# Optimization experiments

Hardware: AMD Instinct MI355X
Metric: run time of the kernel (lower is better)

The kernel has to match this reference:

```python
import jax, jax.numpy as jnp
import numpy as np

Lc, Lq = 20, 50
CTX, CTXM = 2048, 512
NEG = -1e30


def setup_inputs() -> dict:
    key = jax.random.key(0)
    ks = jax.random.split(key, 8)
    B = 2048
    Vid_enc = jax.random.normal(ks[0], (B, Lc, CTX), dtype=jnp.float32)
    Ques_enc = jax.random.normal(ks[1], (B, CTXM, Lq), dtype=jnp.float32)
    V_mask = jnp.ones((B, Lc), dtype=jnp.float32)
    Q_mask = jnp.ones((B, Lq), dtype=jnp.float32)
    # weight-normed Linear(2048 -> 512): v [out,in], g [out], b [out]
    trans_v = jax.random.normal(ks[2], (CTXM, CTX), dtype=jnp.float32) * 0.02
    trans_g = jnp.linalg.norm(trans_v, axis=1)  # matches torch weight_norm init
    trans_b = jnp.zeros((CTXM,), dtype=jnp.float32)
    w4V = jax.random.normal(ks[3], (CTXM, 1), dtype=jnp.float32) * 0.05
    w4Q = jax.random.normal(ks[4], (CTXM, 1), dtype=jnp.float32) * 0.05
    w4mlu = jax.random.normal(ks[5], (1, 1, CTXM), dtype=jnp.float32) * 0.05
    bias = jnp.zeros((1,), dtype=jnp.float32)
    return {
        "Vid_enc": Vid_enc, "Ques_enc": Ques_enc,
        "V_mask": V_mask, "Q_mask": Q_mask,
        "trans_v": trans_v, "trans_g": trans_g, "trans_b": trans_b,
        "w4V": w4V, "w4Q": w4Q, "w4mlu": w4mlu, "bias": bias,
    }


def reference(Vid_enc, Ques_enc, V_mask, Q_mask,
              trans_v, trans_g, trans_b, w4V, w4Q, w4mlu, bias):
    # weight-normed linear projection: W = g * v / ||v||_row
    W = trans_g[:, None] * trans_v / jnp.linalg.norm(trans_v, axis=1, keepdims=True)
    V = jnp.einsum('blc,mc->blm', Vid_enc, W) + trans_b          # [B,Lc,512]
    Q = jnp.swapaxes(Ques_enc, 1, 2)                             # [B,Lq,512]
    # trilinear similarity (dropout p inactive at inference)
    s0 = V @ w4V                                                 # [B,Lc,1]
    s1 = jnp.swapaxes(Q @ w4Q, 1, 2)                             # [B,1,Lq]
    s2 = jnp.einsum('bld,bqd->blq', V * w4mlu, Q)                # [B,Lc,Lq]
    S = s0 + s1 + s2 + bias                                      # [B,Lc,Lq]
    Vm = V_mask[:, :, None]                                      # [B,Lc,1]
    Qm = Q_mask[:, None, :]                                      # [B,1,Lq]
    S1 = jax.nn.softmax(S * Qm + (1.0 - Qm) * NEG, axis=2)
    S2 = jax.nn.softmax(S * Vm + (1.0 - Vm) * NEG, axis=1)
    A = jnp.einsum('blq,bqd->bld', S1, Q)                        # [B,Lc,512]
    Bt = jnp.einsum('blq,bmq->blm', S1, S2)                      # [B,Lc,Lc]
    Bv = jnp.einsum('blm,bmd->bld', Bt, V)                       # [B,Lc,512]
    out = jnp.concatenate([V, A, V * A, V * Bv], axis=2)         # [B,Lc,2048]
    return jnp.swapaxes(out, 1, 2)                               # [B,2048,Lc]
```

## Files before the change

### kernel.cpp

```cpp
#include <hip/hip_runtime.h>
#include <math.h>

#define B_    2048
#define LC    20
#define LQ    50
#define CTX   2048
#define CTXM  512
#define NEGV  -1e30f

typedef __fp16 half8 __attribute__((ext_vector_type(8)));
typedef __fp16 f16x2 __attribute__((ext_vector_type(2)));
typedef float f32x4  __attribute__((ext_vector_type(4)));
typedef unsigned int uint;

__device__ __forceinline__ half8 cvt8v(float4 a, float4 b) {
    union { f16x2 h[4]; half8 v; } r;
    r.h[0] = __builtin_amdgcn_cvt_pkrtz(a.x, a.y);
    r.h[1] = __builtin_amdgcn_cvt_pkrtz(a.z, a.w);
    r.h[2] = __builtin_amdgcn_cvt_pkrtz(b.x, b.y);
    r.h[3] = __builtin_amdgcn_cvt_pkrtz(b.z, b.w);
    return r.v;
}
__device__ __forceinline__ half8 cvt8(const float* x) {
    union { f16x2 h[4]; half8 v; } r;
    r.h[0] = __builtin_amdgcn_cvt_pkrtz(x[0], x[1]);
    r.h[1] = __builtin_amdgcn_cvt_pkrtz(x[2], x[3]);
    r.h[2] = __builtin_amdgcn_cvt_pkrtz(x[4], x[5]);
    r.h[3] = __builtin_amdgcn_cvt_pkrtz(x[6], x[7]);
    return r.v;
}

#define GLOAD_LDS16(g, l)                                                        \
    __builtin_amdgcn_global_load_lds(                                            \
        (const __attribute__((address_space(1))) unsigned int*)(g),              \
        (__attribute__((address_space(3))) unsigned int*)(l), 16, 0, 0)

__global__ __launch_bounds__(256)
void scale_kernel(const float* __restrict__ trans_v,
                  const float* __restrict__ trans_g,
                  float* __restrict__ scale) {
    int m = blockIdx.x;
    int t = threadIdx.x;
    const float* row = trans_v + (size_t)m * CTX;
    float ss = 0.f;
    for (int i = t; i < CTX; i += 256) { float v = row[i]; ss += v * v; }
    __shared__ float red[256];
    red[t] = ss;
    __syncthreads();
    for (int s = 128; s > 0; s >>= 1) {
        if (t < s) red[t] += red[t + s];
        __syncthreads();
    }
    if (t == 0) scale[m] = trans_g[m] / sqrtf(red[0]);
}

__global__ __launch_bounds__(256)
void bpack_kernel(const float* __restrict__ Wt,
                  const float* __restrict__ scale,
                  char* __restrict__ Bp) {
    int u = blockIdx.x * 256 + threadIdx.x;
    int o = u * 16;
    int nslab  = o >> 20;
    int rem    = o & 1048575;
    int kchunk = rem >> 14;
    int rem2   = rem & 16383;
    int rpair  = rem2 >> 7;
    int cphys  = rem2 & 127;
    int clog   = cphys ^ ((rpair & 7) << 4);
    int rsub   = clog >> 6;
    int k0     = kchunk * 32 + ((clog & 63) >> 1);
    int n      = nslab * 256 + rpair * 2 + rsub;
    float s = scale[n];
    const float* wr = Wt + (size_t)n * CTX + k0;
    union { __fp16 h[8]; uint4 u4; } out;
#pragma unroll
    for (int e = 0; e < 8; e++) out.h[e] = (__fp16)(wr[e] * s);
    *(uint4*)&Bp[o] = out.u4;
}

__global__ __launch_bounds__(512, 4)
void gemm_kernel(const float* __restrict__ A,
                 const char*  __restrict__ Bp,
                 const float* __restrict__ trans_b,
                 float* __restrict__ V)
{
    __shared__ char lds[49152] __attribute__((aligned(16)));

    int t = threadIdx.x;
    int orig = blockIdx.x;
    int wg = (orig & 7) * 80 + (orig >> 3);
    int nslab = wg & 1;
    int m0 = (wg >> 1) * 128;
    int n0 = nslab << 8;

    int wid = t >> 6, lane = t & 63;
    int l15 = lane & 15;
    int q16 = (lane >> 4) << 4;
    int ksl = lane >> 4;
    int rq  = (lane >> 4) << 2;
    int wm = (wid >> 2) << 6;
    int wn = (wid & 3) << 6;

    int r_a = t >> 2;
    int sl  = t & 3;
    int a_dst = 32768 + sl * 2048 + r_a * 16;
    const float* arow = A + (size_t)(m0 + r_a) * CTX + sl * 8;

    const char* bslab = Bp + (size_t)nslab * (64 * 16384);

    f32x4 acc[4][4];
#pragma unroll
    for (int i = 0; i < 4; i++)
#pragma unroll
        for (int j = 0; j < 4; j++) acc[i][j] = (f32x4){0.f, 0.f, 0.f, 0.f};

    {
        const char* src = bslab + t * 16;
#pragma unroll
        for (int i = 0; i < 2; i++)
            GLOAD_LDS16(src + i * 8192, lds + i * 8192 + t * 16);
    }
    float4 ra0 = *(const float4*)arow;
    float4 ra1 = *(const float4*)(arow + 4);

    int cur = 0;
    for (int it = 0; it < 64; ++it) {
        *(half8*)&lds[a_dst + cur * 8192] = cvt8v(ra0, ra1);
        __syncthreads();

        if (it + 1 < 64) {
            const char* src = bslab + (size_t)(it + 1) * 16384 + t * 16;
            char* dst = lds + (cur ^ 1) * 16384 + t * 16;
#pragma unroll
            for (int i = 0; i < 2; i++)
                GLOAD_LDS16(src + i * 8192, dst + i * 8192);
            ra0 = *(const float4*)(arow + (it + 1) * 32);
            ra1 = *(const float4*)(arow + (it + 1) * 32 + 4);
        }

        const char* Bb = lds + cur * 16384;
        const char* Ab = lds + 32768 + cur * 8192;
        half8 af[4];
#pragma unroll
        for (int mt = 0; mt < 4; mt++)
            af[mt] = *(const half8*)&Ab[ksl * 2048 + (wm + mt * 16 + l15) * 16];
#pragma unroll
        for (int nt = 0; nt < 4; nt++) {
            int r  = wn + nt * 16 + l15;
            int rp = r >> 1;
            int c  = (r & 1) * 64 + q16;
            half8 bh = *(const half8*)&Bb[rp * 128 + (c ^ ((rp & 7) << 4))];
#pragma unroll
            for (int mt = 0; mt < 4; mt++)
                acc[mt][nt] = __builtin_amdgcn_mfma_f32_16x16x32_f16(af[mt], bh, acc[mt][nt], 0, 0, 0);
        }
        cur ^= 1;
    }

#pragma unroll
    for (int nt = 0; nt < 4; nt++) {
        int col = n0 + wn + nt * 16 + l15;
        float tb = trans_b[col];
#pragma unroll
        for (int mt = 0; mt < 4; mt++) {
            int m = m0 + wm + mt * 16 + rq;
#pragma unroll
            for (int rg = 0; rg < 4; rg++)
                V[(size_t)(m + rg) * CTXM + col] = acc[mt][nt][rg] + tb;
        }
    }
}

__global__ __launch_bounds__(512, 2)
void attn_kernel(const float* __restrict__ Ques,
                 const float* __restrict__ V_mask,
                 const float* __restrict__ Q_mask,
                 const float* __restrict__ w4V,
                 const float* __restrict__ w4Q,
                 const float* __restrict__ w4mlu,
                 const float* __restrict__ bias,
                 const float* __restrict__ V,
                 float* __restrict__ out)
{
    __shared__ __fp16 Qs[512 * 56 + 8];
    __shared__ float Ssh[LC][LQ];
    __shared__ float S1f[LC][LQ];
    __shared__ float S2f[LC][LQ];
    __shared__ __fp16 S1h[LC][72];
    __shared__ __fp16 S1l[LC][72];
    __shared__ __fp16 Bth[LC][40];
    __shared__ __fp16 Btl[LC][40];
    __shared__ float s1p[8][LQ];
    __shared__ float s0sh[LC];
    __shared__ float s1qsh[LQ];
    __shared__ float qmsh[LQ];
    __shared__ float vmsh[LC];

    int b = blockIdx.x;
    int t = threadIdx.x;
    int wid = t >> 6, lane = t & 63;
    int l15 = lane & 15;
    int kq  = (lane >> 4) << 3;
    int rq  = (lane >> 4) << 2;
    const float* Qb = Ques + (size_t)b * (CTXM * LQ);
    const float* Vb = V + (size_t)b * (LC * CTXM);

    if (t < LQ) qmsh[t] = Q_mask[(size_t)b * LQ + t];
    else if (t >= 64 && t < 64 + LC) vmsh[t - 64] = V_mask[(size_t)b * LC + (t - 64)];
    if (t < 8) Qs[512 * 56 + t] = (__fp16)0;

#pragma unroll
    for (int i = 0; i < 7; i++) {
        int task = t + 512 * i;
        int d  = task / 7;
        int sc = task - d * 7;
        const float* qr = Qb + (size_t)d * LQ + sc * 8;
        float xs[8];
        if (sc < 6) {
            float2 p0 = *(const float2*)&qr[0];
            float2 p1 = *(const float2*)&qr[2];
            float2 p2 = *(const float2*)&qr[4];
            float2 p3 = *(const float2*)&qr[6];
            xs[0] = p0.x; xs[1] = p0.y; xs[2] = p1.x; xs[3] = p1.y;
            xs[4] = p2.x; xs[5] = p2.y; xs[6] = p3.x; xs[7] = p3.y;
        } else {
            float2 p0 = *(const float2*)&qr[0];
            xs[0] = p0.x; xs[1] = p0.y;
            xs[2] = 0.f; xs[3] = 0.f; xs[4] = 0.f; xs[5] = 0.f;
            xs[6] = 0.f; xs[7] = 0.f;
        }
        *(half8*)&Qs[d * 56 + sc * 8] = cvt8(xs);
    }

    for (int l = wid; l < LC; l += 8) {
        float a = 0.f;
        const float* vr = Vb + (size_t)l * CTXM;
#pragma unroll
        for (int i = 0; i < CTXM / 64; i++)
            a = fmaf(vr[lane + 64 * i], w4V[lane + 64 * i], a);
#pragma unroll
        for (int o = 32; o > 0; o >>= 1) a += __shfl_xor(a, o);
        if (lane == 0) s0sh[l] = a;
    }
    __syncthreads();

    {
        int q = (lane < LQ) ? lane : (LQ - 1);
        float a = 0.f;
#pragma unroll
        for (int i = 0; i < 64; i++) {
            int d = (wid << 6) + i;
            a = fmaf((float)Qs[d * 56 + q], w4Q[d], a);
        }
        if (lane < LQ) s1p[wid][lane] = a;
    }

    int mt = wid >> 2, nt = wid & 3;
    f32x4 accS = {0.f, 0.f, 0.f, 0.f};
    {
        int lA = mt * 16 + l15; if (lA > LC - 1) lA = LC - 1;
        int qB = nt * 16 + l15; if (qB > LQ - 1) qB = LQ - 1;
        const float* vrow = Vb + (size_t)lA * CTXM;
        for (int kt = 0; kt < 16; kt++) {
            int d0 = kt * 32 + kq;
            float xa[8];
            float4 va = *(const float4*)&vrow[d0];
            float4 vc = *(const float4*)&vrow[d0 + 4];
            float4 wa = *(const float4*)&w4mlu[d0];
            float4 wc = *(const float4*)&w4mlu[d0 + 4];
            xa[0] = va.x * wa.x; xa[1] = va.y * wa.y; xa[2] = va.z * wa.z; xa[3] = va.w * wa.w;
            xa[4] = vc.x * wc.x; xa[5] = vc.y * wc.y; xa[6] = vc.z * wc.z; xa[7] = vc.w * wc.w;
            half8 vf = cvt8(xa);
            union { __fp16 h[8]; half8 v; } qq;
#pragma unroll
            for (int e = 0; e < 8; e++) qq.h[e] = Qs[(d0 + e) * 56 + qB];
            accS = __builtin_amdgcn_mfma_f32_16x16x32_f16(vf, qq.v, accS, 0, 0, 0);
        }
    }
    __syncthreads();

    if (t < LQ) {
        float s = 0.f;
#pragma unroll
        for (int w = 0; w < 8; w++) s += s1p[w][t];
        s1qsh[t] = s;
    }
    __syncthreads();

    {
        float bb = bias[0];
        int q = nt * 16 + l15;
#pragma unroll
        for (int r = 0; r < 4; r++) {
            int l = mt * 16 + rq + r;
            if (l < LC && q < LQ)
                Ssh[l][q] = accS[r] + s0sh[l] + s1qsh[q] + bb;
        }
    }
    __syncthreads();

    for (int l = wid; l < LC; l += 8) {
        float x;
        if (lane < LQ) {
            float qm = qmsh[lane];
            x = Ssh[l][lane] * qm + (1.f - qm) * NEGV;
        } else x = -INFINITY;
        float mx = x;
#pragma unroll
        for (int o = 32; o > 0; o >>= 1) mx = fmaxf(mx, __shfl_xor(mx, o));
        float e = (lane < LQ) ? expf(x - mx) : 0.f;
        float sum = e;
#pragma unroll
        for (int o = 32; o > 0; o >>= 1) sum += __shfl_xor(sum, o);
        float p = e / sum;
        if (lane < LQ) S1f[l][lane] = p;
        __fp16 hs = (__fp16)p;
        __fp16 ls = (__fp16)(p - (float)hs);
        S1h[l][lane] = (lane < LQ) ? hs : (__fp16)0;
        S1l[l][lane] = (lane < LQ) ? ls : (__fp16)0;
    }

    for (int ci = 0; ci < 7; ci++) {
        int c = wid * 7 + ci;
        if (c < LQ) {
            float x;
            if (lane < LC) {
                float vm = vmsh[lane];
                x = Ssh[lane][c] * vm + (1.f - vm) * NEGV;
            } else x = -INFINITY;
            float mx = x;
#pragma unroll
            for (int o = 32; o > 0; o >>= 1) mx = fmaxf(mx, __shfl_xor(mx, o));
            float e = (lane < LC) ? expf(x - mx) : 0.f;
            float sum = e;
#pragma unroll
            for (int o = 32; o > 0; o >>= 1) sum += __shfl_xor(sum, o);
            if (lane < LC) S2f[lane][c] = e / sum;
        }
    }
    __syncthreads();

    if (t < LC * LC) {
        int l = t % LC, m = t / LC;
        float s = 0.f;
#pragma unroll
        for (int j = 0; j < LQ; j++) s = fmaf(S1f[l][j], S2f[m][j], s);
        __fp16 hs = (__fp16)s;
        Bth[l][m] = hs;
        Btl[l][m] = (__fp16)(s - (float)hs);
    }
    if (t < 240) {
        int l = t % LC, m = LC + t / LC;
        Bth[l][m] = (__fp16)0; Btl[l][m] = (__fp16)0;
    }
    __syncthreads();

    float* outb = out + (size_t)b * (4 * CTXM * LC);
#pragma unroll 1
    for (int i = 0; i < 4; i++) {
        int dt = wid + 8 * i;
        int d0 = dt * 16;
        int dq = d0 + l15;
        half8 qf0 = *(const half8*)&Qs[dq * 56 + kq];
        half8 qf1 = *(const half8*)&Qs[dq * 56 + 32 + kq];
        float xv[8];
#pragma unroll
        for (int e = 0; e < 8; e++) {
            int m = kq + e;
            int mc = (m < LC) ? m : 0;
            float vv = Vb[(size_t)mc * CTXM + d0 + l15];
            xv[e] = (m < LC) ? vv : 0.f;
        }
        half8 vt = cvt8(xv);

        f32x4 accA[2] = {{0.f,0.f,0.f,0.f},{0.f,0.f,0.f,0.f}};
        f32x4 accB[2] = {{0.f,0.f,0.f,0.f},{0.f,0.f,0.f,0.f}};
#pragma unroll
        for (int n2 = 0; n2 < 2; n2++) {
            int lS = n2 * 16 + l15; if (lS > LC - 1) lS = LC - 1;
            half8 s1h0 = *(const half8*)&S1h[lS][kq];
            half8 s1l0 = *(const half8*)&S1l[lS][kq];
            half8 s1h1 = *(const half8*)&S1h[lS][32 + kq];
            half8 s1l1 = *(const half8*)&S1l[lS][32 + kq];
            accA[n2] = __builtin_amdgcn_mfma_f32_16x16x32_f16(qf0, s1h0, accA[n2], 0, 0, 0);
            accA[n2] = __builtin_amdgcn_mfma_f32_16x16x32_f16(qf0, s1l0, accA[n2], 0, 0, 0);
            accA[n2] = __builtin_amdgcn_mfma_f32_16x16x32_f16(qf1, s1h1, accA[n2], 0, 0, 0);
            accA[n2] = __builtin_amdgcn_mfma_f32_16x16x32_f16(qf1, s1l1, accA[n2], 0, 0, 0);
            half8 bh = *(const half8*)&Bth[lS][kq];
            half8 bl = *(const half8*)&Btl[lS][kq];
            accB[n2] = __builtin_amdgcn_mfma_f32_16x16x32_f16(vt, bh, accB[n2], 0, 0, 0);
            accB[n2] = __builtin_amdgcn_mfma_f32_16x16x32_f16(vt, bl, accB[n2], 0, 0, 0);
        }

#pragma unroll
        for (int n2 = 0; n2 < 2; n2++) {
            int l = n2 * 16 + l15;
            if (l < LC) {
#pragma unroll
                for (int r = 0; r < 4; r++) {
                    int d = d0 + rq + r;
                    float vv = Vb[(size_t)l * CTXM + d];
                    float a  = accA[n2][r];
                    float bv = accB[n2][r];
                    size_t base = (size_t)d * LC + l;
                    outb[base]                 = vv;
                    outb[base + CTXM * LC]     = a;
                    outb[base + 2 * CTXM * LC] = vv * a;
                    outb[base + 3 * CTXM * LC] = vv * bv;
                }
            }
        }
    }
}

extern "C" void kernel_launch(void* const* d_in, const int* in_sizes, int n_in,
                              void* d_out, int out_size, void* d_ws, size_t ws_size,
                              hipStream_t stream) {
    const float* Vid   = (const float*)d_in[0];
    const float* Ques  = (const float*)d_in[1];
    const float* Vmask = (const float*)d_in[2];
    const float* Qmask = (const float*)d_in[3];
    const float* tv    = (const float*)d_in[4];
    const float* tg    = (const float*)d_in[5];
    const float* tb    = (const float*)d_in[6];
    const float* w4V   = (const float*)d_in[7];
    const float* w4Q   = (const float*)d_in[8];
    const float* w4mlu = (const float*)d_in[9];
    const float* bias  = (const float*)d_in[10];
    float* out = (float*)d_out;

    float* scale = (float*)d_ws;
    float* V     = scale + 512;
    char*  Bp    = (char*)(V + (size_t)40960 * 512);

    scale_kernel<<<512, 256, 0, stream>>>(tv, tg, scale);
    bpack_kernel<<<512, 256, 0, stream>>>(tv, scale, Bp);
    gemm_kernel<<<640, 512, 0, stream>>>(Vid, Bp, tb, V);
    attn_kernel<<<B_, 512, 0, stream>>>(Ques, Vmask, Qmask, w4V, w4Q, w4mlu, bias, V, out);
}
```

Before: 401.0 us.

## Unroll GEMM k-loop by two with explicit vmcnt waits and raw barriers

Rewrites the projection GEMM main loop to process two k-steps per iteration with fixed LDS buffer offsets. It replaces __syncthreads with s_barrier plus explicit s_waitcnt vmcnt(2), so async global-to-LDS loads for the next stage stay in flight across the barrier instead of being fully drained. The A-tile register prefetch now reaches one stage further ahead. The hand-counted waits depend on the exact order of memory ops, which makes the code fragile if the compiler reorders loads.

```diff
diff --git a/kernel.cpp b/kernel.cpp
--- a/kernel.cpp
+++ b/kernel.cpp
@@ -116,45 +116,83 @@
 
     {
         const char* src = bslab + t * 16;
-#pragma unroll
-        for (int i = 0; i < 2; i++)
-            GLOAD_LDS16(src + i * 8192, lds + i * 8192 + t * 16);
-    }
-    float4 ra0 = *(const float4*)arow;
-    float4 ra1 = *(const float4*)(arow + 4);
-
-    int cur = 0;
-    for (int it = 0; it < 64; ++it) {
-        *(half8*)&lds[a_dst + cur * 8192] = cvt8v(ra0, ra1);
-        __syncthreads();
-
-        if (it + 1 < 64) {
-            const char* src = bslab + (size_t)(it + 1) * 16384 + t * 16;
-            char* dst = lds + (cur ^ 1) * 16384 + t * 16;
-#pragma unroll
-            for (int i = 0; i < 2; i++)
-                GLOAD_LDS16(src + i * 8192, dst + i * 8192);
-            ra0 = *(const float4*)(arow + (it + 1) * 32);
-            ra1 = *(const float4*)(arow + (it + 1) * 32 + 4);
-        }
-
-        const char* Bb = lds + cur * 16384;
-        const char* Ab = lds + 32768 + cur * 8192;
-        half8 af[4];
-#pragma unroll
-        for (int mt = 0; mt < 4; mt++)
-            af[mt] = *(const half8*)&Ab[ksl * 2048 + (wm + mt * 16 + l15) * 16];
-#pragma unroll
-        for (int nt = 0; nt < 4; nt++) {
-            int r  = wn + nt * 16 + l15;
-            int rp = r >> 1;
-            int c  = (r & 1) * 64 + q16;
-            half8 bh = *(const half8*)&Bb[rp * 128 + (c ^ ((rp & 7) << 4))];
+        GLOAD_LDS16(src, lds + t * 16);
+        GLOAD_LDS16(src + 8192, lds + 8192 + t * 16);
+    }
+    float4 rAe0 = *(const float4*)(arow);
+    float4 rAe1 = *(const float4*)(arow + 4);
+    float4 rAo0 = *(const float4*)(arow + 32);
+    float4 rAo1 = *(const float4*)(arow + 36);
+
+    for (int ii = 0; ii < 32; ++ii) {
+        int t0 = ii * 2;
+        *(half8*)&lds[a_dst] = cvt8v(rAe0, rAe1);
+        asm volatile("s_waitcnt vmcnt(2)" ::: "memory");
+        asm volatile("s_waitcnt lgkmcnt(0)" ::: "memory");
+        __builtin_amdgcn_sched_barrier(0);
+        __builtin_amdgcn_s_barrier();
+        __builtin_amdgcn_sched_barrier(0);
+        {
+            const char* src = bslab + (size_t)(t0 + 1) * 16384 + t * 16;
+            GLOAD_LDS16(src, lds + 16384 + t * 16);
+            GLOAD_LDS16(src + 8192, lds + 16384 + 8192 + t * 16);
+        }
+        if (ii < 31) {
+            rAe0 = *(const float4*)(arow + (size_t)(t0 + 2) * 32);
+            rAe1 = *(const float4*)(arow + (size_t)(t0 + 2) * 32 + 4);
+        }
+        {
+            const char* Bb = lds;
+            const char* Ab = lds + 32768;
+            half8 af[4];
 #pragma unroll
             for (int mt = 0; mt < 4; mt++)
-                acc[mt][nt] = __builtin_amdgcn_mfma_f32_16x16x32_f16(af[mt], bh, acc[mt][nt], 0, 0, 0);
-        }
-        cur ^= 1;
+                af[mt] = *(const half8*)&Ab[ksl * 2048 + (wm + mt * 16 + l15) * 16];
+#pragma unroll
+            for (int nt = 0; nt < 4; nt++) {
+                int r  = wn + nt * 16 + l15;
+                int rp = r >> 1;
+                int c  = (r & 1) * 64 + q16;
+                half8 bh = *(const half8*)&Bb[rp * 128 + (c ^ ((rp & 7) << 4))];
+#pragma unroll
+                for (int mt = 0; mt < 4; mt++)
+                    acc[mt][nt] = __builtin_amdgcn_mfma_f32_16x16x32_f16(af[mt], bh, acc[mt][nt], 0, 0, 0);
+            }
+        }
+        *(half8*)&lds[a_dst + 8192] = cvt8v(rAo0, rAo1);
+        if (ii < 31) asm volatile("s_waitcnt vmcnt(2)" ::: "memory");
+        else         asm volatile("s_waitcnt vmcnt(0)" ::: "memory");
+        asm volatile("s_waitcnt lgkmcnt(0)" ::: "memory");
+        __builtin_amdgcn_sched_barrier(0);
+        __builtin_amdgcn_s_barrier();
+        __builtin_amdgcn_sched_barrier(0);
+        if (ii < 31) {
+            {
+                const char* src = bslab + (size_t)(t0 + 2) * 16384 + t * 16;
+                GLOAD_LDS16(src, lds + t * 16);
+                GLOAD_LDS16(src + 8192, lds + 8192 + t * 16);
+            }
+            rAo0 = *(const float4*)(arow + (size_t)(t0 + 3) * 32);
+            rAo1 = *(const float4*)(arow + (size_t)(t0 + 3) * 32 + 4);
+        }
+        {
+            const char* Bb = lds + 16384;
+            const char* Ab = lds + 32768 + 8192;
+            half8 af[4];
+#pragma unroll
+            for (int mt = 0; mt < 4; mt++)
+                af[mt] = *(const half8*)&Ab[ksl * 2048 + (wm + mt * 16 + l15) * 16];
+#pragma unroll
+            for (int nt = 0; nt < 4; nt++) {
+                int r  = wn + nt * 16 + l15;
+                int rp = r >> 1;
+                int c  = (r & 1) * 64 + q16;
+                half8 bh = *(const half8*)&Bb[rp * 128 + (c ^ ((rp & 7) << 4))];
+#pragma unroll
+                for (int mt = 0; mt < 4; mt++)
+                    acc[mt][nt] = __builtin_amdgcn_mfma_f32_16x16x32_f16(af[mt], bh, acc[mt][nt], 0, 0, 0);
+            }
+        }
     }
 
 #pragma unroll
```

New measurement: 369.7 us, median of 2. 7.8% less time.
